# Kernel tuning notes

Measured on AMD Instinct MI355X. Metric: run time of the kernel, lower is better.

## Reference

```python
import jax, jax.numpy as jnp
import numpy as np
from jax import lax

SR = 4      # sr_ratio
HEADS = 8   # num_heads


def _upsample_bilinear_ac(x, out_h, out_w):
    # torch nn.Upsample(scale_factor=SR, mode='bilinear', align_corners=True)
    B, C, h, w = x.shape
    ys = jnp.linspace(0.0, h - 1.0, out_h)
    xs = jnp.linspace(0.0, w - 1.0, out_w)
    y0 = jnp.floor(ys).astype(jnp.int32)
    y1 = jnp.minimum(y0 + 1, h - 1)
    wy = (ys - y0).astype(x.dtype)
    x0 = jnp.floor(xs).astype(jnp.int32)
    x1 = jnp.minimum(x0 + 1, w - 1)
    wx = (xs - x0).astype(x.dtype)
    r = x[:, :, y0, :] * (1.0 - wy)[None, None, :, None] + x[:, :, y1, :] * wy[None, None, :, None]
    return r[:, :, :, x0] * (1.0 - wx) + r[:, :, :, x1] * wx


def _forward(x, sr_w, sr_b, ln_g, ln_b, q_w, k1_w, v1_w, k2_w, v2_w, proj_w, proj_b):
    B, C, H, W = x.shape
    ID = C // 4                      # internal_dim
    hd = ID // HEADS                 # head_dim
    scale = float(hd) ** -0.5
    # spatial-reduction conv for Q path: [B, ID, H/4, W/4]
    qf = lax.conv_general_dilated(x, sr_w, (SR, SR), 'VALID',
                                  dimension_numbers=('NCHW', 'OIHW', 'NCHW'))
    qf = qf + sr_b[None, :, None, None]
    Hs, Ws = qf.shape[2], qf.shape[3]
    N = Hs * Ws
    qf = qf.reshape(B, ID, N).transpose(0, 2, 1)          # [B, N, ID]
    # LayerNorm
    mu = qf.mean(-1, keepdims=True)
    var = qf.var(-1, keepdims=True)
    qn = (qf - mu) / jnp.sqrt(var + 1e-5) * ln_g + ln_b
    q = qn @ q_w                                          # [B, N, ID]
    # max / avg pooled K,V inputs: [B, N, C]
    xm = lax.reduce_window(x, -jnp.inf, lax.max, (1, 1, SR, SR), (1, 1, SR, SR), 'VALID')
    xm = xm.reshape(B, C, N).transpose(0, 2, 1)
    xa = lax.reduce_window(x, 0.0, lax.add, (1, 1, SR, SR), (1, 1, SR, SR), 'VALID') / float(SR * SR)
    xa = xa.reshape(B, C, N).transpose(0, 2, 1)

    def heads(t):
        return t.reshape(B, N, HEADS, hd).transpose(0, 2, 1, 3)  # [B, H, N, hd]

    qh = heads(q)
    k1, v1 = heads(xm @ k1_w), heads(xm @ v1_w)
    k2, v2 = heads(xa @ k2_w), heads(xa @ v2_w)

    def attend(k, v):
        a = jax.nn.softmax(jnp.einsum('bhnd,bhmd->bhnm', qh, k) * scale, axis=-1)
        return jnp.einsum('bhnm,bhmd->bhnd', a, v)

    z = attend(k1, v1) + attend(k2, v2)                   # [B, H, N, hd]
    z = z.transpose(0, 2, 1, 3).reshape(B, N, ID)
    z = z @ proj_w + proj_b                               # [B, N, C]
    z = z.transpose(0, 2, 1).reshape(B, C, Hs, Ws)
    return _upsample_bilinear_ac(z, H, W)


def setup_inputs() -> dict:
    key = jax.random.key(0)
    ks = jax.random.split(key, 9)
    B, C, H, W = 16, 256, 112, 112
    ID = C // 4

    def n(k, shape, s=0.02):
        return jax.random.normal(k, shape, jnp.float32) * s

    return {
        'x': jax.random.normal(ks[0], (B, C, H, W), jnp.float32),
        'sr_w': n(ks[1], (ID, C, SR, SR)),
        'sr_b': jnp.zeros((ID,), jnp.float32),
        'ln_g': jnp.ones((ID,), jnp.float32),
        'ln_b': jnp.zeros((ID,), jnp.float32),
        'q_w': n(ks[2], (ID, ID)),
        'k1_w': n(ks[3], (C, ID)),
        'v1_w': n(ks[4], (C, ID)),
        'k2_w': n(ks[5], (C, ID)),
        'v2_w': n(ks[6], (C, ID)),
        'proj_w': n(ks[7], (ID, C)),
        'proj_b': jnp.zeros((C,), jnp.float32),
    }


def reference(x, sr_w, sr_b, ln_g, ln_b, q_w, k1_w, v1_w, k2_w, v2_w, proj_w, proj_b):
    return _forward(x, sr_w, sr_b, ln_g, ln_b, q_w, k1_w, v1_w, k2_w, v2_w, proj_w, proj_b)
```

## Files before the change

### kernel.cpp

```cpp
#include <hip/hip_runtime.h>
#include <math.h>

typedef __attribute__((ext_vector_type(8))) short short8;
typedef __attribute__((ext_vector_type(4))) short bh4;
typedef __attribute__((ext_vector_type(4))) float f32x4;
typedef __attribute__((ext_vector_type(2))) unsigned uint2v;

#define MFMA16(A,B,C) __builtin_amdgcn_mfma_f32_16x16x32_bf16(A,B,C,0,0,0)

#if __has_builtin(__builtin_amdgcn_mfma_f32_16x16x16bf16_1k)
#define MFMA16x16(A,B,C) __builtin_amdgcn_mfma_f32_16x16x16bf16_1k(A,B,C,0,0,0)
#else
__device__ __forceinline__ f32x4 mfma16x16_asm(bh4 a, bh4 b, f32x4 c){
    asm volatile("v_mfma_f32_16x16x16_bf16 %0, %1, %2, %0" : "+v"(c) : "v"(a), "v"(b));
    return c;
}
#define MFMA16x16(A,B,C) mfma16x16_asm(A,B,C)
#endif

__device__ __forceinline__ unsigned short f2b(float f){
    unsigned u = __builtin_bit_cast(unsigned, f);
    return (unsigned short)((u + 0x7fffu + ((u>>16)&1u)) >> 16);
}
__device__ __forceinline__ unsigned pk2(float a, float b){
    return (unsigned)f2b(a) | ((unsigned)f2b(b) << 16);
}
__device__ __forceinline__ unsigned pk2rn(float a, float b){
    unsigned ua = __builtin_bit_cast(unsigned, a) + 0x8000u;
    unsigned ub = __builtin_bit_cast(unsigned, b) + 0x8000u;
    return (ua >> 16) | (ub & 0xffff0000u);
}
__device__ __forceinline__ float b2f_lo(unsigned u){ return __builtin_bit_cast(float, u << 16); }
__device__ __forceinline__ float b2f_hi(unsigned u){ return __builtin_bit_cast(float, u & 0xffff0000u); }


__global__ __launch_bounds__(256) void ktw(const float* __restrict__ srw,
    const float* __restrict__ qw, const float* __restrict__ k1w,
    const float* __restrict__ v1w, const float* __restrict__ k2w,
    const float* __restrict__ v2w, char* __restrict__ srwb,
    char* __restrict__ Wtm, char* __restrict__ Wta, char* __restrict__ QWt)
{
    int blk = blockIdx.x, t = threadIdx.x;
    if (blk < 128){
        int base = blk*2048 + t*8;
        float4 a = *(const float4*)(srw + base);
        float4 b = *(const float4*)(srw + base + 4);
        uint4 u = { pk2(a.x,a.y), pk2(a.z,a.w), pk2(b.x,b.y), pk2(b.z,b.w) };
        *(uint4*)(srwb + (size_t)base*2) = u;
    } else if (blk < 136){
        __shared__ float T[256*33];
        int idx = blk - 128, fi = idx >> 1, half = idx & 1;
        const float* src = (fi==0) ? k1w : (fi==1) ? v1w : (fi==2) ? k2w : v2w;
        char* dst = ((fi < 2) ? Wtm : Wta) + (size_t)((fi & 1)*64 + half*32) * 512;
        for (int li = t; li < 8192; li += 256){
            int c = li >> 5, o = li & 31;
            T[c*33 + o] = src[c*64 + half*32 + o];
        }
        __syncthreads();
        for (int lo = t; lo < 1024; lo += 256){
            int o = lo >> 5, c8 = lo & 31;
            float v[8];
            #pragma unroll
            for (int k = 0; k < 8; ++k) v[k] = T[(c8*8 + k)*33 + o];
            uint4 u = { pk2(v[0],v[1]), pk2(v[2],v[3]), pk2(v[4],v[5]), pk2(v[6],v[7]) };
            *(uint4*)(dst + o*512 + c8*16) = u;
        }
    } else {
        __shared__ float T[64*65];
        for (int li = t; li < 4096; li += 256)
            T[(li >> 6)*65 + (li & 63)] = qw[li];
        __syncthreads();
        for (int lo = t; lo < 512; lo += 256){
            int o = lo >> 3, i8 = lo & 7;
            float v[8];
            #pragma unroll
            for (int k = 0; k < 8; ++k) v[k] = T[(i8*8 + k)*65 + o];
            uint4 u = { pk2(v[0],v[1]), pk2(v[2],v[3]), pk2(v[4],v[5]), pk2(v[6],v[7]) };
            *(uint4*)(QWt + o*128 + i8*16) = u;
        }
    }
}

__global__ __launch_bounds__(512) void k1(const float* __restrict__ x,
    const char* __restrict__ srwb, char* __restrict__ R, float* __restrict__ pws)
{
    __shared__ __align__(16) char A[32768];
    __shared__ float pm[28*33 + 4];
    __shared__ float pa[28*33 + 4];
    int blk = blockIdx.x;
    int b = blk / 56, r5 = blk % 56, hs = r5 >> 1, cgp = r5 & 1;
    int t = threadIdx.x;
    int w = t >> 6, l = t & 63, lr = l & 15, lg = l >> 4;
    int ofr = w & 3, mfr = w >> 2;
    int c0 = t / 28, p = t % 28;
    f32x4 acc = {0.f,0.f,0.f,0.f};
    const char* Brow = srwb + (size_t)(ofr*16 + lr)*8192 + cgp*4096;
    size_t rowB = (size_t)b*784 + hs*28;

    for (int ci = 0; ci < 4; ++ci){
        int cg = cgp*4 + ci;
        __syncthreads();
        if (t < 448){
            #pragma unroll
            for (int kk = 0; kk < 2; ++kk){
                int c = c0 + kk*16;
                const float* base = x + ((size_t)(b*256 + cg*32 + c)*112 + hs*4)*112 + p*4;
                float4 v0 = *(const float4*)(base);
                float4 v1 = *(const float4*)(base + 112);
                float4 v2 = *(const float4*)(base + 224);
                float4 v3 = *(const float4*)(base + 336);
                float mx = fmaxf(fmaxf(fmaxf(v0.x,v0.y),fmaxf(v0.z,v0.w)),
                                 fmaxf(fmaxf(v1.x,v1.y),fmaxf(v1.z,v1.w)));
                mx = fmaxf(mx, fmaxf(fmaxf(fmaxf(v2.x,v2.y),fmaxf(v2.z,v2.w)),
                                     fmaxf(fmaxf(v3.x,v3.y),fmaxf(v3.z,v3.w))));
                float sm = (v0.x+v0.y+v0.z+v0.w)+(v1.x+v1.y+v1.z+v1.w)
                         + (v2.x+v2.y+v2.z+v2.w)+(v3.x+v3.y+v3.z+v3.w);
                pm[p*33 + c] = mx;
                pa[p*33 + c] = sm * (1.f/16.f);
                char* Ap = A + p*1024;
                int swz = (p & 7) << 4;
                uint2 u0 = { pk2(v0.x,v0.y), pk2(v0.z,v0.w) };
                uint2 u1 = { pk2(v1.x,v1.y), pk2(v1.z,v1.w) };
                uint2 u2 = { pk2(v2.x,v2.y), pk2(v2.z,v2.w) };
                uint2 u3 = { pk2(v3.x,v3.y), pk2(v3.z,v3.w) };
                *(uint2*)(Ap + ((c*32 +  0) ^ swz)) = u0;
                *(uint2*)(Ap + ((c*32 +  8) ^ swz)) = u1;
                *(uint2*)(Ap + ((c*32 + 16) ^ swz)) = u2;
                *(uint2*)(Ap + ((c*32 + 24) ^ swz)) = u3;
            }
        }
        __syncthreads();
        if (t < 112){
            int m = t >> 2, c8 = t & 3;
            float vm[8], va8[8];
            #pragma unroll
            for (int k = 0; k < 8; ++k){
                vm[k]  = pm[m*33 + c8*8 + k];
                va8[k] = pa[m*33 + c8*8 + k];
            }
            uint4 um = { pk2(vm[0],vm[1]), pk2(vm[2],vm[3]), pk2(vm[4],vm[5]), pk2(vm[6],vm[7]) };
            uint4 ua = { pk2(va8[0],va8[1]), pk2(va8[2],va8[3]), pk2(va8[4],va8[5]), pk2(va8[6],va8[7]) };
            *(uint4*)(R + (rowB + m)*1024 + cg*64 + c8*16)       = um;
            *(uint4*)(R + (rowB + m)*1024 + 512 + cg*64 + c8*16) = ua;
        }
        const char* Arow = A + (mfr*16 + lr)*1024;
        const char* Bc = Brow + ci*1024;
        int swzr = (lr & 7) << 4;
        #pragma unroll
        for (int ks = 0; ks < 16; ++ks){
            int kb = ks*64 + lg*16;
            short8 a  = *(const short8*)(Arow + (kb ^ swzr));
            short8 bf = *(const short8*)(Bc + kb);
            acc = MFMA16(a, bf, acc);
        }
    }
    float* pp = pws + (size_t)((b*28 + hs)*2 + cgp)*1792;
    #pragma unroll
    for (int rg = 0; rg < 4; ++rg){
        int m = mfr*16 + lg*4 + rg;
        if (m < 28) pp[m*64 + ofr*16 + lr] = acc[rg];
    }
}

__global__ __launch_bounds__(512) void k2(const float* __restrict__ pws_,
    const float* __restrict__ srb, const float* __restrict__ lng,
    const float* __restrict__ lnb, const char* __restrict__ Wtm,
    const char* __restrict__ Wta, const char* __restrict__ QWt,
    char* __restrict__ R)
{
    __shared__ __align__(16) char PM[16384];
    __shared__ __align__(16) char PA[16384];
    __shared__ float Db[32*64];
    __shared__ __align__(16) char QN[4096];
    int blk = blockIdx.x, b = blk/28, hs = blk%28;
    int t = threadIdx.x, w = t>>6, l = t&63, lr = l&15, lg = l>>4;
    size_t rowB = (size_t)b*784 + hs*28;
    const char* Rb = R + rowB*1024;
    for (int li = t; li < 896; li += 512){
        int m = li >> 5, c16 = li & 31;
        uint4 vm = *(const uint4*)(Rb + (size_t)m*1024 + c16*16);
        uint4 va = *(const uint4*)(Rb + (size_t)m*1024 + 512 + c16*16);
        int dst = m*512 + ((c16*16) ^ ((m&7)<<4));
        *(uint4*)(PM + dst) = vm;
        *(uint4*)(PA + dst) = va;
    }
    const float* p0 = pws_ + (size_t)(b*28 + hs)*2*1792;
    const float* p1 = p0 + 1792;
    for (int e = t; e < 1792; e += 512)
        Db[e] = p0[e] + p1[e] + srb[e & 63];
    __syncthreads();
    float g = lng[l], be = lnb[l];
    #pragma unroll
    for (int i = 0; i < 4; ++i){
        int m = w + i*8;
        float v = Db[m*64 + l];
        float s = v, ss = v*v;
        #pragma unroll
        for (int off = 1; off < 64; off <<= 1){
            s  += __shfl_xor(s,  off, 64);
            ss += __shfl_xor(ss, off, 64);
        }
        float mu = s * (1.f/64.f);
        float var = ss * (1.f/64.f) - mu*mu;
        float qn = (v - mu) * rsqrtf(var + 1e-5f) * g + be;
        *(unsigned short*)(QN + m*128 + ((l*2) ^ ((m&7)<<4))) = f2b(qn);
    }
    __syncthreads();
    int fam = w >> 2, ofp = w & 3;
    const char* PMA = fam ? PA : PM;
    const char* Wt  = fam ? Wta : Wtm;
    f32x4 a00={0.f,0.f,0.f,0.f}, a01=a00, a10=a00, a11=a00;
    int swzr = (lr & 7) << 4;
    #pragma unroll
    for (int ks = 0; ks < 8; ++ks){
        int kb = ks*64 + lg*16;
        short8 x0 = *(const short8*)(PMA + lr*512 + (kb ^ swzr));
        short8 x1 = *(const short8*)(PMA + (16+lr)*512 + (kb ^ swzr));
        short8 b0 = *(const short8*)(Wt + (size_t)(ofp*32 + lr)*512 + kb);
        short8 b1 = *(const short8*)(Wt + (size_t)(ofp*32 + 16 + lr)*512 + kb);
        a00 = MFMA16(x0, b0, a00); a01 = MFMA16(x0, b1, a01);
        a10 = MFMA16(x1, b0, a10); a11 = MFMA16(x1, b1, a11);
    }
    f32x4 q0={0.f,0.f,0.f,0.f}, q1=q0;
    if (w < 4){
        #pragma unroll
        for (int ks = 0; ks < 2; ++ks){
            int kb = ks*64 + lg*16;
            short8 xa_ = *(const short8*)(QN + lr*128 + (kb ^ swzr));
            short8 xb_ = *(const short8*)(QN + (16+lr)*128 + (kb ^ swzr));
            short8 bq  = *(const short8*)(QWt + (size_t)(w*16 + lr)*128 + kb);
            q0 = MFMA16(xa_, bq, q0);
            q1 = MFMA16(xb_, bq, q1);
        }
    }
    #pragma unroll
    for (int j = 0; j < 2; ++j){
        int o128 = ofp*32 + j*16 + lr;
        int o = o128 & 63, hh = o >> 3, dd = o & 7, mat = fam*2 + (o128 >> 6);
        int byteoff = 128 + hh*64 + mat*16 + dd*2;
        f32x4 am  = j ? a01 : a00;
        f32x4 am1 = j ? a11 : a10;
        #pragma unroll
        for (int rg = 0; rg < 4; ++rg){
            int m0 = lg*4 + rg, m1 = 16 + lg*4 + rg;
            *(unsigned short*)(R + (rowB + m0)*1024 + byteoff) = f2b(am[rg]);
            if (m1 < 28)
                *(unsigned short*)(R + (rowB + m1)*1024 + byteoff) = f2b(am1[rg]);
        }
    }
    if (w < 4){
        int o = w*16 + lr;
        #pragma unroll
        for (int rg = 0; rg < 4; ++rg){
            int m0 = lg*4 + rg, m1 = 16 + lg*4 + rg;
            *(unsigned short*)(R + (rowB + m0)*1024 + o*2) = f2b(q0[rg]);
            if (m1 < 28)
                *(unsigned short*)(R + (rowB + m1)*1024 + o*2) = f2b(q1[rg]);
        }
    }
}

__global__ __launch_bounds__(256) void kattn(const char* __restrict__ R, float* __restrict__ z)
{
    __shared__ __align__(16) char QT [6144];
    __shared__ __align__(16) char K1b[5376];
    __shared__ __align__(16) char K2b[5376];
    __shared__ __align__(16) char VT1[3840];
    __shared__ __align__(16) char VT2[3840];
    int blk = blockIdx.x;
    int bh = blk / 7, nseg = blk % 7;
    int b = bh >> 3, h = bh & 7;
    int t = threadIdx.x, w = t >> 6, l = t & 63;
    int col = l & 15, g = l >> 4;

    for (int i = t; i < 384; i += 256) ((uint4*)QT)[i] = uint4{0,0,0,0};
    for (int i = t; i < 112; i += 256){
        *(uint4*)(K1b + i*48 + 16) = uint4{0,0,0,0};
        *(uint4*)(K2b + i*48 + 16) = uint4{0,0,0,0};
    }
    for (int i = t; i < 120; i += 256){
        *(uint4*)(VT1 + 1920 + i*16) = uint4{0,0,0,0};
        *(uint4*)(VT2 + 1920 + i*16) = uint4{0,0,0,0};
    }
    __syncthreads();
    if (t < 112){
        uint4 qv = *(const uint4*)(R + ((size_t)b*784 + nseg*112 + t)*1024 + h*16);
        *(uint2*)(QT + t*48)     = uint2{qv.x, qv.y};
        *(uint2*)(QT + t*48 + 8) = uint2{qv.z, qv.w};
    }
    __syncthreads();

    bh4 qf[2];
    #pragma unroll
    for (int nf = 0; nf < 2; ++nf)
        qf[nf] = *(const bh4*)(QT + (w*28 + nf*16 + col)*48 + g*8);

    f32x4 o1[2] = {{0,0,0,0},{0,0,0,0}}, o2[2] = {{0,0,0,0},{0,0,0,0}};
    float d1[2] = {0.f,0.f}, d2[2] = {0.f,0.f};
    const float C2 = 0.51004244f;

    for (int mt = 0; mt < 7; ++mt){
        __syncthreads();
        for (int li = t; li < 448; li += 256){
            int m = li >> 2, part = li & 3;
            uint4 v = *(const uint4*)(R + ((size_t)b*784 + mt*112 + m)*1024 + 128 + h*64 + part*16);
            if ((part & 1) == 0){
                char* Kb = (part == 0) ? K1b : K2b;
                *(uint2*)(Kb + m*48)     = uint2{v.x, v.y};
                *(uint2*)(Kb + m*48 + 8) = uint2{v.z, v.w};
            } else {
                char* Vb = (part == 1) ? VT1 : VT2;
                unsigned arr[4] = {v.x, v.y, v.z, v.w};
                #pragma unroll
                for (int d = 0; d < 4; ++d){
                    *(unsigned short*)(Vb + (d*2)*240   + m*2) = (unsigned short)(arr[d] & 0xffffu);
                    *(unsigned short*)(Vb + (d*2+1)*240 + m*2) = (unsigned short)(arr[d] >> 16);
                }
            }
        }
        __syncthreads();
        #pragma unroll
        for (int mc = 0; mc < 7; ++mc){
            bh4 ka = *(const bh4*)(K1b + (mc*16 + col)*48 + g*8);
            bh4 kb = *(const bh4*)(K2b + (mc*16 + col)*48 + g*8);
            bh4 va = *(const bh4*)(VT1 + col*240 + mc*32 + g*8);
            bh4 vb = *(const bh4*)(VT2 + col*240 + mc*32 + g*8);
            #pragma unroll
            for (int nf = 0; nf < 2; ++nf){
                f32x4 zr = {0.f,0.f,0.f,0.f};
                f32x4 s1 = MFMA16x16(ka, qf[nf], zr);
                float p0 = exp2f(s1[0]*C2), p1 = exp2f(s1[1]*C2);
                float p2 = exp2f(s1[2]*C2), p3 = exp2f(s1[3]*C2);
                d1[nf] += (p0+p1)+(p2+p3);
                bh4 pf1 = __builtin_bit_cast(bh4, (uint2v){pk2rn(p0,p1), pk2rn(p2,p3)});
                o1[nf] = MFMA16x16(va, pf1, o1[nf]);
                f32x4 s2 = MFMA16x16(kb, qf[nf], zr);
                float r0 = exp2f(s2[0]*C2), r1 = exp2f(s2[1]*C2);
                float r2 = exp2f(s2[2]*C2), r3 = exp2f(s2[3]*C2);
                d2[nf] += (r0+r1)+(r2+r3);
                bh4 pf2 = __builtin_bit_cast(bh4, (uint2v){pk2rn(r0,r1), pk2rn(r2,r3)});
                o2[nf] = MFMA16x16(vb, pf2, o2[nf]);
            }
        }
    }
    #pragma unroll
    for (int nf = 0; nf < 2; ++nf){
        d1[nf] += __shfl_xor(d1[nf], 16, 64); d1[nf] += __shfl_xor(d1[nf], 32, 64);
        d2[nf] += __shfl_xor(d2[nf], 16, 64); d2[nf] += __shfl_xor(d2[nf], 32, 64);
    }
    if (g < 2){
        #pragma unroll
        for (int nf = 0; nf < 2; ++nf){
            if (nf == 1 && col >= 12) continue;
            int n = nseg*112 + w*28 + nf*16 + col;
            float ra = 1.f / d1[nf], rb = 1.f / d2[nf];
            float4 ov;
            ov.x = o1[nf][0]*ra + o2[nf][0]*rb;
            ov.y = o1[nf][1]*ra + o2[nf][1]*rb;
            ov.z = o1[nf][2]*ra + o2[nf][2]*rb;
            ov.w = o1[nf][3]*ra + o2[nf][3]*rb;
            *(float4*)(z + ((size_t)b*784 + n)*64 + h*8 + g*4) = ov;
        }
    }
}

__global__ __launch_bounds__(256) void kproj(const float* __restrict__ z,
    const float* __restrict__ pw, const float* __restrict__ pb,
    float* __restrict__ zc)
{
    __shared__ float zs[28*64];
    int blk = blockIdx.x;
    int b = blk / 28, hs = blk % 28;
    int t = threadIdx.x;
    const float* zrow = z + ((size_t)b*784 + hs*28)*64;
    for (int li = t; li < 1792; li += 256) zs[li] = zrow[li];
    __syncthreads();
    int c = t;
    float acc[28];
    float bias = pb[c];
    #pragma unroll
    for (int wsI = 0; wsI < 28; ++wsI) acc[wsI] = bias;
    for (int o = 0; o < 64; ++o){
        float wv = pw[o*256 + c];
        #pragma unroll
        for (int wsI = 0; wsI < 28; ++wsI) acc[wsI] = fmaf(zs[wsI*64+o], wv, acc[wsI]);
    }
    float* op = zc + (((size_t)(b*256 + c))*28 + hs)*28;
    #pragma unroll
    for (int f = 0; f < 7; ++f)
        ((float4*)op)[f] = make_float4(acc[4*f], acc[4*f+1], acc[4*f+2], acc[4*f+3]);
}

__global__ __launch_bounds__(256) void kups(const float* __restrict__ zc, float* __restrict__ out)
{
    __shared__ float plane[784];
    __shared__ int   ti0[112];
    __shared__ float twv[112];
    int bc = blockIdx.x;
    int t = threadIdx.x;
    const float* src = zc + (size_t)bc*784;
    for (int li = t; li < 784; li += 256) plane[li] = src[li];
    if (t < 112){
        float s = (float)t * (27.f/111.f);
        int i0 = (int)s;
        if (i0 > 27) i0 = 27;
        ti0[t] = i0;
        twv[t] = s - (float)i0;
    }
    __syncthreads();
    float* op = out + (size_t)bc*12544;
    for (int i = t; i < 12544; i += 256){
        int y = i/112, xx = i%112;
        int y0 = ti0[y], x0 = ti0[xx];
        float wy = twv[y], wx = twv[xx];
        int y1 = min(y0+1, 27), x1 = min(x0+1, 27);
        const float* r0 = plane + y0*28;
        const float* r1 = plane + y1*28;
        float a  = r0[x0] + (r1[x0]-r0[x0])*wy;
        float bb = r0[x1] + (r1[x1]-r0[x1])*wy;
        op[i] = a + (bb-a)*wx;
    }
}

extern "C" void kernel_launch(void* const* d_in, const int* in_sizes, int n_in,
                              void* d_out, int out_size, void* d_ws, size_t ws_size,
                              hipStream_t stream) {
    const float* x   = (const float*)d_in[0];
    const float* srw = (const float*)d_in[1];
    const float* srb = (const float*)d_in[2];
    const float* lng = (const float*)d_in[3];
    const float* lnb = (const float*)d_in[4];
    const float* qw  = (const float*)d_in[5];
    const float* k1w = (const float*)d_in[6];
    const float* v1w = (const float*)d_in[7];
    const float* k2w = (const float*)d_in[8];
    const float* v2w = (const float*)d_in[9];
    const float* pw  = (const float*)d_in[10];
    const float* pb  = (const float*)d_in[11];

    char*  Rws  = (char*)d_ws;
    float* pws  = (float*)(Rws + 12845056);
    char*  srwb = Rws + 19267584;
    char*  Wtm  = Rws + 19791872;
    char*  Wta  = Rws + 19857408;
    char*  QWt  = Rws + 19922944;
    float* z    = (float*)(Rws + 12845056);
    float* zc   = z + 802816;
    float* out  = (float*)d_out;

    ktw  <<<137, 256, 0, stream>>>(srw, qw, k1w, v1w, k2w, v2w, srwb, Wtm, Wta, QWt);
    k1   <<<896, 512, 0, stream>>>(x, srwb, Rws, pws);
    k2   <<<448, 512, 0, stream>>>(pws, srb, lng, lnb, Wtm, Wta, QWt, Rws);
    kattn<<<896, 256, 0, stream>>>(Rws, z);
    kproj<<<448, 256, 0, stream>>>(z, pw, pb, zc);
    kups <<<4096, 256, 0, stream>>>(zc, out);
}
```

Before: 270.4 us.

## Double-buffer k1 LDS tiles and prefetch next x/weight chunk into registers

Restructures the k1 conv/pooling loop into a manually unrolled, double-buffered pipeline. The next channel group's x tile and bf16 weights are loaded into registers while the current buffer feeds the MFMAs, which cuts the syncthreads per iteration to one. The aim is to hide global load latency behind the matrix work. In exchange it doubles LDS use to about 72KB and raises register pressure (16 float4 plus 32 short8), which may lower occupancy.

```diff
diff --git a/kernel.cpp b/kernel.cpp
--- a/kernel.cpp
+++ b/kernel.cpp
@@ -32,7 +32,6 @@
 }
 __device__ __forceinline__ float b2f_lo(unsigned u){ return __builtin_bit_cast(float, u << 16); }
 __device__ __forceinline__ float b2f_hi(unsigned u){ return __builtin_bit_cast(float, u & 0xffff0000u); }
-
 
 __global__ __launch_bounds__(256) void ktw(const float* __restrict__ srw,
     const float* __restrict__ qw, const float* __restrict__ k1w,
@@ -84,76 +83,105 @@
 __global__ __launch_bounds__(512) void k1(const float* __restrict__ x,
     const char* __restrict__ srwb, char* __restrict__ R, float* __restrict__ pws)
 {
-    __shared__ __align__(16) char A[32768];
-    __shared__ float pm[28*33 + 4];
-    __shared__ float pa[28*33 + 4];
+    __shared__ __align__(16) char Ab[2][32768];
+    __shared__ float pm[2][924];
+    __shared__ float pa[2][924];
     int blk = blockIdx.x;
     int b = blk / 56, r5 = blk % 56, hs = r5 >> 1, cgp = r5 & 1;
     int t = threadIdx.x;
     int w = t >> 6, l = t & 63, lr = l & 15, lg = l >> 4;
     int ofr = w & 3, mfr = w >> 2;
     int c0 = t / 28, p = t % 28;
+    bool ldr = t < 448;
     f32x4 acc = {0.f,0.f,0.f,0.f};
     const char* Brow = srwb + (size_t)(ofr*16 + lr)*8192 + cgp*4096;
     size_t rowB = (size_t)b*784 + hs*28;
-
-    for (int ci = 0; ci < 4; ++ci){
-        int cg = cgp*4 + ci;
-        __syncthreads();
-        if (t < 448){
-            #pragma unroll
-            for (int kk = 0; kk < 2; ++kk){
-                int c = c0 + kk*16;
-                const float* base = x + ((size_t)(b*256 + cg*32 + c)*112 + hs*4)*112 + p*4;
-                float4 v0 = *(const float4*)(base);
-                float4 v1 = *(const float4*)(base + 112);
-                float4 v2 = *(const float4*)(base + 224);
-                float4 v3 = *(const float4*)(base + 336);
-                float mx = fmaxf(fmaxf(fmaxf(v0.x,v0.y),fmaxf(v0.z,v0.w)),
-                                 fmaxf(fmaxf(v1.x,v1.y),fmaxf(v1.z,v1.w)));
-                mx = fmaxf(mx, fmaxf(fmaxf(fmaxf(v2.x,v2.y),fmaxf(v2.z,v2.w)),
-                                     fmaxf(fmaxf(v3.x,v3.y),fmaxf(v3.z,v3.w))));
-                float sm = (v0.x+v0.y+v0.z+v0.w)+(v1.x+v1.y+v1.z+v1.w)
-                         + (v2.x+v2.y+v2.z+v2.w)+(v3.x+v3.y+v3.z+v3.w);
-                pm[p*33 + c] = mx;
-                pa[p*33 + c] = sm * (1.f/16.f);
-                char* Ap = A + p*1024;
-                int swz = (p & 7) << 4;
-                uint2 u0 = { pk2(v0.x,v0.y), pk2(v0.z,v0.w) };
-                uint2 u1 = { pk2(v1.x,v1.y), pk2(v1.z,v1.w) };
-                uint2 u2 = { pk2(v2.x,v2.y), pk2(v2.z,v2.w) };
-                uint2 u3 = { pk2(v3.x,v3.y), pk2(v3.z,v3.w) };
-                *(uint2*)(Ap + ((c*32 +  0) ^ swz)) = u0;
-                *(uint2*)(Ap + ((c*32 +  8) ^ swz)) = u1;
-                *(uint2*)(Ap + ((c*32 + 16) ^ swz)) = u2;
-                *(uint2*)(Ap + ((c*32 + 24) ^ swz)) = u3;
-            }
-        }
-        __syncthreads();
-        if (t < 112){
-            int m = t >> 2, c8 = t & 3;
-            float vm[8], va8[8];
-            #pragma unroll
-            for (int k = 0; k < 8; ++k){
-                vm[k]  = pm[m*33 + c8*8 + k];
-                va8[k] = pa[m*33 + c8*8 + k];
-            }
-            uint4 um = { pk2(vm[0],vm[1]), pk2(vm[2],vm[3]), pk2(vm[4],vm[5]), pk2(vm[6],vm[7]) };
-            uint4 ua = { pk2(va8[0],va8[1]), pk2(va8[2],va8[3]), pk2(va8[4],va8[5]), pk2(va8[6],va8[7]) };
-            *(uint4*)(R + (rowB + m)*1024 + cg*64 + c8*16)       = um;
-            *(uint4*)(R + (rowB + m)*1024 + 512 + cg*64 + c8*16) = ua;
-        }
-        const char* Arow = A + (mfr*16 + lr)*1024;
-        const char* Bc = Brow + ci*1024;
-        int swzr = (lr & 7) << 4;
-        #pragma unroll
-        for (int ks = 0; ks < 16; ++ks){
-            int kb = ks*64 + lg*16;
-            short8 a  = *(const short8*)(Arow + (kb ^ swzr));
-            short8 bf = *(const short8*)(Bc + kb);
-            acc = MFMA16(a, bf, acc);
-        }
-    }
+    const float* xpb = x + (size_t)(b*256 + cgp*128)*12544 + hs*4*112 + p*4;
+    int swzp = (p & 7) << 4;
+    int swzr = (lr & 7) << 4;
+
+    float4 xr0[8], xr1[8];
+    short8 bf0[16], bf1[16];
+
+#define LOADX(XR, CI) do { if (ldr){ \
+    const float* _s0 = xpb + (size_t)((CI)*32 + c0)*12544; \
+    const float* _s1 = _s0 + (size_t)16*12544; \
+    XR[0]=*(const float4*)(_s0);     XR[1]=*(const float4*)(_s0+112); \
+    XR[2]=*(const float4*)(_s0+224); XR[3]=*(const float4*)(_s0+336); \
+    XR[4]=*(const float4*)(_s1);     XR[5]=*(const float4*)(_s1+112); \
+    XR[6]=*(const float4*)(_s1+224); XR[7]=*(const float4*)(_s1+336); } } while(0)
+
+#define LOADB(BF, CI) do { _Pragma("unroll") \
+    for (int ks = 0; ks < 16; ++ks) \
+        BF[ks] = *(const short8*)(Brow + (CI)*1024 + ks*64 + lg*16); } while(0)
+
+#define WRITEA(BUF, XR) do { if (ldr){ \
+    _Pragma("unroll") \
+    for (int kk = 0; kk < 2; ++kk){ \
+        float4 v0 = XR[kk*4+0], v1 = XR[kk*4+1], v2 = XR[kk*4+2], v3 = XR[kk*4+3]; \
+        float mx = fmaxf(fmaxf(fmaxf(v0.x,v0.y),fmaxf(v0.z,v0.w)), \
+                         fmaxf(fmaxf(v1.x,v1.y),fmaxf(v1.z,v1.w))); \
+        mx = fmaxf(mx, fmaxf(fmaxf(fmaxf(v2.x,v2.y),fmaxf(v2.z,v2.w)), \
+                             fmaxf(fmaxf(v3.x,v3.y),fmaxf(v3.z,v3.w)))); \
+        float sm = (v0.x+v0.y+v0.z+v0.w)+(v1.x+v1.y+v1.z+v1.w) \
+                 + (v2.x+v2.y+v2.z+v2.w)+(v3.x+v3.y+v3.z+v3.w); \
+        int c = c0 + kk*16; \
+        pm[BUF][p*33 + c] = mx; \
+        pa[BUF][p*33 + c] = sm * (1.f/16.f); \
+        char* Ap = Ab[BUF] + p*1024; \
+        *(uint2*)(Ap + ((c*32 +  0) ^ swzp)) = (uint2){ pk2(v0.x,v0.y), pk2(v0.z,v0.w) }; \
+        *(uint2*)(Ap + ((c*32 +  8) ^ swzp)) = (uint2){ pk2(v1.x,v1.y), pk2(v1.z,v1.w) }; \
+        *(uint2*)(Ap + ((c*32 + 16) ^ swzp)) = (uint2){ pk2(v2.x,v2.y), pk2(v2.z,v2.w) }; \
+        *(uint2*)(Ap + ((c*32 + 24) ^ swzp)) = (uint2){ pk2(v3.x,v3.y), pk2(v3.z,v3.w) }; \
+    } } } while(0)
+
+#define POOLW(BUF, CI) do { if (t < 112){ \
+    int m_ = t >> 2, c8 = t & 3; \
+    float vm[8], va8[8]; \
+    _Pragma("unroll") \
+    for (int kq = 0; kq < 8; ++kq){ \
+        vm[kq]  = pm[BUF][m_*33 + c8*8 + kq]; \
+        va8[kq] = pa[BUF][m_*33 + c8*8 + kq]; } \
+    uint4 um = { pk2(vm[0],vm[1]), pk2(vm[2],vm[3]), pk2(vm[4],vm[5]), pk2(vm[6],vm[7]) }; \
+    uint4 ua = { pk2(va8[0],va8[1]), pk2(va8[2],va8[3]), pk2(va8[4],va8[5]), pk2(va8[6],va8[7]) }; \
+    int cg = cgp*4 + (CI); \
+    *(uint4*)(R + (rowB + m_)*1024 + cg*64 + c8*16)       = um; \
+    *(uint4*)(R + (rowB + m_)*1024 + 512 + cg*64 + c8*16) = ua; } } while(0)
+
+#define MFMAPH(BUF, BF) do { \
+    const char* Arow = Ab[BUF] + (mfr*16 + lr)*1024; \
+    _Pragma("unroll") \
+    for (int ks = 0; ks < 16; ++ks){ \
+        short8 a = *(const short8*)(Arow + ((ks*64 + lg*16) ^ swzr)); \
+        acc = MFMA16(a, BF[ks], acc); } } while(0)
+
+    LOADX(xr0, 0); LOADB(bf0, 0);
+
+    WRITEA(0, xr0);
+    LOADX(xr1, 1); LOADB(bf1, 1);
+    __syncthreads();
+    POOLW(0, 0); MFMAPH(0, bf0);
+
+    WRITEA(1, xr1);
+    LOADX(xr0, 2); LOADB(bf0, 2);
+    __syncthreads();
+    POOLW(1, 1); MFMAPH(1, bf1);
+
+    WRITEA(0, xr0);
+    LOADX(xr1, 3); LOADB(bf1, 3);
+    __syncthreads();
+    POOLW(0, 2); MFMAPH(0, bf0);
+
+    WRITEA(1, xr1);
+    __syncthreads();
+    POOLW(1, 3); MFMAPH(1, bf1);
+
+#undef LOADX
+#undef LOADB
+#undef WRITEA
+#undef POOLW
+#undef MFMAPH
+
     float* pp = pws + (size_t)((b*28 + hs)*2 + cgp)*1792;
     #pragma unroll
     for (int rg = 0; rg < 4; ++rg){
```

New measurement: 262.3 us. -3.0%, faster.

## Load conv operands directly into MFMA registers and split k1 over four channel groups

Applied to the files above, without the earlier changes.

The k1 conv+pooling kernel no longer stages the bf16 input tile in LDS. Each lane loads float4 rows straight from global memory, packs them into MFMA A fragments, and computes max/avg pooling with a cross-lane shuffle. The grid is split into four 64-channel groups with 256-thread blocks, which doubles the block count and removes most of the syncthreads. k2 now sums four partial results instead of two, and the workspace offsets are moved to fit the larger partial buffer. Every one of the four waves reloads the same x data, so redundant global/L2 reads go up in exchange for less LDS traffic and fewer barriers.

```diff
diff --git a/kernel.cpp b/kernel.cpp
--- a/kernel.cpp
+++ b/kernel.cpp
@@ -5,6 +5,7 @@
 typedef __attribute__((ext_vector_type(4))) short bh4;
 typedef __attribute__((ext_vector_type(4))) float f32x4;
 typedef __attribute__((ext_vector_type(2))) unsigned uint2v;
+typedef __attribute__((ext_vector_type(4))) unsigned uint4v;
 
 #define MFMA16(A,B,C) __builtin_amdgcn_mfma_f32_16x16x32_bf16(A,B,C,0,0,0)
 
@@ -30,8 +31,6 @@
     unsigned ub = __builtin_bit_cast(unsigned, b) + 0x8000u;
     return (ua >> 16) | (ub & 0xffff0000u);
 }
-__device__ __forceinline__ float b2f_lo(unsigned u){ return __builtin_bit_cast(float, u << 16); }
-__device__ __forceinline__ float b2f_hi(unsigned u){ return __builtin_bit_cast(float, u & 0xffff0000u); }
 
 
 __global__ __launch_bounds__(256) void ktw(const float* __restrict__ srw,
@@ -81,84 +80,75 @@
     }
 }
 
-__global__ __launch_bounds__(512) void k1(const float* __restrict__ x,
+__global__ __launch_bounds__(256) void k1(const float* __restrict__ x,
     const char* __restrict__ srwb, char* __restrict__ R, float* __restrict__ pws)
 {
-    __shared__ __align__(16) char A[32768];
-    __shared__ float pm[28*33 + 4];
-    __shared__ float pa[28*33 + 4];
+    __shared__ float pm[28*66];
+    __shared__ float pa[28*66];
     int blk = blockIdx.x;
-    int b = blk / 56, r5 = blk % 56, hs = r5 >> 1, cgp = r5 & 1;
+    int b = blk / 112, r5 = blk % 112, hs = r5 >> 2, cg4 = r5 & 3;
     int t = threadIdx.x;
     int w = t >> 6, l = t & 63, lr = l & 15, lg = l >> 4;
-    int ofr = w & 3, mfr = w >> 2;
-    int c0 = t / 28, p = t % 28;
-    f32x4 acc = {0.f,0.f,0.f,0.f};
-    const char* Brow = srwb + (size_t)(ofr*16 + lr)*8192 + cgp*4096;
+    int cpar = lg >> 1, r0 = (lg & 1) * 2;
+    f32x4 acc0 = {0.f,0.f,0.f,0.f}, acc1 = {0.f,0.f,0.f,0.f};
+    const float* xc = x + (size_t)(b*256 + cg4*64)*12544 + (size_t)(hs*4 + r0)*112;
+    const char* Brow = srwb + (size_t)(w*16 + lr)*8192 + cg4*2048 + lg*16;
+    int p0 = lr, p1 = min(16 + lr, 27);
     size_t rowB = (size_t)b*784 + hs*28;
 
-    for (int ci = 0; ci < 4; ++ci){
-        int cg = cgp*4 + ci;
-        __syncthreads();
-        if (t < 448){
-            #pragma unroll
-            for (int kk = 0; kk < 2; ++kk){
-                int c = c0 + kk*16;
-                const float* base = x + ((size_t)(b*256 + cg*32 + c)*112 + hs*4)*112 + p*4;
-                float4 v0 = *(const float4*)(base);
-                float4 v1 = *(const float4*)(base + 112);
-                float4 v2 = *(const float4*)(base + 224);
-                float4 v3 = *(const float4*)(base + 336);
-                float mx = fmaxf(fmaxf(fmaxf(v0.x,v0.y),fmaxf(v0.z,v0.w)),
-                                 fmaxf(fmaxf(v1.x,v1.y),fmaxf(v1.z,v1.w)));
-                mx = fmaxf(mx, fmaxf(fmaxf(fmaxf(v2.x,v2.y),fmaxf(v2.z,v2.w)),
-                                     fmaxf(fmaxf(v3.x,v3.y),fmaxf(v3.z,v3.w))));
-                float sm = (v0.x+v0.y+v0.z+v0.w)+(v1.x+v1.y+v1.z+v1.w)
-                         + (v2.x+v2.y+v2.z+v2.w)+(v3.x+v3.y+v3.z+v3.w);
-                pm[p*33 + c] = mx;
-                pa[p*33 + c] = sm * (1.f/16.f);
-                char* Ap = A + p*1024;
-                int swz = (p & 7) << 4;
-                uint2 u0 = { pk2(v0.x,v0.y), pk2(v0.z,v0.w) };
-                uint2 u1 = { pk2(v1.x,v1.y), pk2(v1.z,v1.w) };
-                uint2 u2 = { pk2(v2.x,v2.y), pk2(v2.z,v2.w) };
-                uint2 u3 = { pk2(v3.x,v3.y), pk2(v3.z,v3.w) };
-                *(uint2*)(Ap + ((c*32 +  0) ^ swz)) = u0;
-                *(uint2*)(Ap + ((c*32 +  8) ^ swz)) = u1;
-                *(uint2*)(Ap + ((c*32 + 16) ^ swz)) = u2;
-                *(uint2*)(Ap + ((c*32 + 24) ^ swz)) = u3;
+    #pragma unroll 8
+    for (int ks = 0; ks < 32; ++ks){
+        const float* s = xc + (size_t)(ks*2 + cpar)*12544;
+        float4 a0r0 = *(const float4*)(s + p0*4);
+        float4 a0r1 = *(const float4*)(s + 112 + p0*4);
+        float4 a1r0 = *(const float4*)(s + p1*4);
+        float4 a1r1 = *(const float4*)(s + 112 + p1*4);
+        short8 bf = *(const short8*)(Brow + ks*64);
+        if (w == 0){
+            float mx0 = fmaxf(fmaxf(fmaxf(a0r0.x,a0r0.y),fmaxf(a0r0.z,a0r0.w)),
+                              fmaxf(fmaxf(a0r1.x,a0r1.y),fmaxf(a0r1.z,a0r1.w)));
+            float sm0 = (a0r0.x+a0r0.y)+(a0r0.z+a0r0.w)+(a0r1.x+a0r1.y)+(a0r1.z+a0r1.w);
+            float mx1 = fmaxf(fmaxf(fmaxf(a1r0.x,a1r0.y),fmaxf(a1r0.z,a1r0.w)),
+                              fmaxf(fmaxf(a1r1.x,a1r1.y),fmaxf(a1r1.z,a1r1.w)));
+            float sm1 = (a1r0.x+a1r0.y)+(a1r0.z+a1r0.w)+(a1r1.x+a1r1.y)+(a1r1.z+a1r1.w);
+            mx0 = fmaxf(mx0, __shfl_xor(mx0, 16, 64));
+            sm0 = sm0 + __shfl_xor(sm0, 16, 64);
+            mx1 = fmaxf(mx1, __shfl_xor(mx1, 16, 64));
+            sm1 = sm1 + __shfl_xor(sm1, 16, 64);
+            if ((lg & 1) == 0){
+                int c = ks*2 + cpar;
+                pm[p0*66 + c] = mx0; pa[p0*66 + c] = sm0 * (1.f/16.f);
+                if (lr < 12){ pm[p1*66 + c] = mx1; pa[p1*66 + c] = sm1 * (1.f/16.f); }
             }
         }
-        __syncthreads();
-        if (t < 112){
-            int m = t >> 2, c8 = t & 3;
-            float vm[8], va8[8];
-            #pragma unroll
-            for (int k = 0; k < 8; ++k){
-                vm[k]  = pm[m*33 + c8*8 + k];
-                va8[k] = pa[m*33 + c8*8 + k];
-            }
-            uint4 um = { pk2(vm[0],vm[1]), pk2(vm[2],vm[3]), pk2(vm[4],vm[5]), pk2(vm[6],vm[7]) };
-            uint4 ua = { pk2(va8[0],va8[1]), pk2(va8[2],va8[3]), pk2(va8[4],va8[5]), pk2(va8[6],va8[7]) };
-            *(uint4*)(R + (rowB + m)*1024 + cg*64 + c8*16)       = um;
-            *(uint4*)(R + (rowB + m)*1024 + 512 + cg*64 + c8*16) = ua;
-        }
-        const char* Arow = A + (mfr*16 + lr)*1024;
-        const char* Bc = Brow + ci*1024;
-        int swzr = (lr & 7) << 4;
-        #pragma unroll
-        for (int ks = 0; ks < 16; ++ks){
-            int kb = ks*64 + lg*16;
-            short8 a  = *(const short8*)(Arow + (kb ^ swzr));
-            short8 bf = *(const short8*)(Bc + kb);
-            acc = MFMA16(a, bf, acc);
-        }
-    }
-    float* pp = pws + (size_t)((b*28 + hs)*2 + cgp)*1792;
+        short8 af0 = __builtin_bit_cast(short8,
+            (uint4v){ pk2(a0r0.x,a0r0.y), pk2(a0r0.z,a0r0.w), pk2(a0r1.x,a0r1.y), pk2(a0r1.z,a0r1.w) });
+        short8 af1 = __builtin_bit_cast(short8,
+            (uint4v){ pk2(a1r0.x,a1r0.y), pk2(a1r0.z,a1r0.w), pk2(a1r1.x,a1r1.y), pk2(a1r1.z,a1r1.w) });
+        acc0 = MFMA16(af0, bf, acc0);
+        acc1 = MFMA16(af1, bf, acc1);
+    }
+
+    float* pp = pws + (size_t)((b*28 + hs)*4 + cg4)*1792;
     #pragma unroll
     for (int rg = 0; rg < 4; ++rg){
-        int m = mfr*16 + lg*4 + rg;
-        if (m < 28) pp[m*64 + ofr*16 + lr] = acc[rg];
+        int m0 = lg*4 + rg, m1 = 16 + lg*4 + rg;
+        pp[m0*64 + w*16 + lr] = acc0[rg];
+        if (m1 < 28) pp[m1*64 + w*16 + lr] = acc1[rg];
+    }
+    __syncthreads();
+    if (t < 224){
+        int m = t >> 3, sub = t & 7;
+        float vm[8], va8[8];
+        #pragma unroll
+        for (int k = 0; k < 8; ++k){
+            vm[k]  = pm[m*66 + sub*8 + k];
+            va8[k] = pa[m*66 + sub*8 + k];
+        }
+        uint4 um = { pk2(vm[0],vm[1]), pk2(vm[2],vm[3]), pk2(vm[4],vm[5]), pk2(vm[6],vm[7]) };
+        uint4 ua = { pk2(va8[0],va8[1]), pk2(va8[2],va8[3]), pk2(va8[4],va8[5]), pk2(va8[6],va8[7]) };
+        *(uint4*)(R + (rowB + m)*1024 + cg4*128 + sub*16)       = um;
+        *(uint4*)(R + (rowB + m)*1024 + 512 + cg4*128 + sub*16) = ua;
     }
 }
 
@@ -184,10 +174,9 @@
         *(uint4*)(PM + dst) = vm;
         *(uint4*)(PA + dst) = va;
     }
-    const float* p0 = pws_ + (size_t)(b*28 + hs)*2*1792;
-    const float* p1 = p0 + 1792;
+    const float* p0 = pws_ + (size_t)(b*28 + hs)*4*1792;
     for (int e = t; e < 1792; e += 512)
-        Db[e] = p0[e] + p1[e] + srb[e & 63];
+        Db[e] = ((p0[e] + p0[1792+e]) + (p0[3584+e] + p0[5376+e])) + srb[e & 63];
     __syncthreads();
     float g = lng[l], be = lnb[l];
     #pragma unroll
@@ -440,18 +429,18 @@
 
     char*  Rws  = (char*)d_ws;
     float* pws  = (float*)(Rws + 12845056);
-    char*  srwb = Rws + 19267584;
-    char*  Wtm  = Rws + 19791872;
-    char*  Wta  = Rws + 19857408;
-    char*  QWt  = Rws + 19922944;
+    char*  srwb = Rws + 25690112;
+    char*  Wtm  = Rws + 26214400;
+    char*  Wta  = Rws + 26279936;
+    char*  QWt  = Rws + 26345472;
     float* z    = (float*)(Rws + 12845056);
-    float* zc   = z + 802816;
+    float* zc   = (float*)(Rws + 16056320);
     float* out  = (float*)d_out;
 
-    ktw  <<<137, 256, 0, stream>>>(srw, qw, k1w, v1w, k2w, v2w, srwb, Wtm, Wta, QWt);
-    k1   <<<896, 512, 0, stream>>>(x, srwb, Rws, pws);
-    k2   <<<448, 512, 0, stream>>>(pws, srb, lng, lnb, Wtm, Wta, QWt, Rws);
-    kattn<<<896, 256, 0, stream>>>(Rws, z);
-    kproj<<<448, 256, 0, stream>>>(z, pw, pb, zc);
+    ktw  <<<137,  256, 0, stream>>>(srw, qw, k1w, v1w, k2w, v2w, srwb, Wtm, Wta, QWt);
+    k1   <<<1792, 256, 0, stream>>>(x, srwb, Rws, pws);
+    k2   <<<448,  512, 0, stream>>>(pws, srb, lng, lnb, Wtm, Wta, QWt, Rws);
+    kattn<<<896,  256, 0, stream>>>(Rws, z);
+    kproj<<<448,  256, 0, stream>>>(z, pw, pb, zc);
     kups <<<4096, 256, 0, stream>>>(zc, out);
 }
```

Measured after the change: 284.4 us. 1.05x slower.
